# Kernel optimization log

Hardware: AMD Instinct MI355X
Metric: run time of the kernel (lower is better)

Reference implementation:

```python
import jax, jax.numpy as jnp
import numpy as np

NUM_NODES = 100000
HIDDEN = 128
NUM_EDGES = 800000


def setup_inputs() -> dict:
    key = jax.random.key(0)
    ks = jax.random.split(key, 8)
    s = 1.0 / np.sqrt(HIDDEN)

    def lin_w(k):
        return jax.random.uniform(k, (HIDDEN, HIDDEN), minval=-s, maxval=s, dtype=jnp.float32)

    return {
        "node_id": jnp.arange(NUM_NODES, dtype=jnp.int64) if jax.config.jax_enable_x64 else jnp.arange(NUM_NODES, dtype=jnp.int32),
        "edge_index": jax.random.randint(ks[0], (2, NUM_EDGES), 0, NUM_NODES),
        "emb": jax.random.normal(ks[1], (NUM_NODES, HIDDEN), dtype=jnp.float32),
        "W1l": lin_w(ks[2]), "b1l": jnp.zeros((HIDDEN,), jnp.float32), "W1r": lin_w(ks[3]),
        "W2l": lin_w(ks[4]), "b2l": jnp.zeros((HIDDEN,), jnp.float32), "W2r": lin_w(ks[5]),
        "W3l": lin_w(ks[6]), "b3l": jnp.zeros((HIDDEN,), jnp.float32), "W3r": lin_w(ks[7]),
    }


def reference(node_id, edge_index, emb, W1l, b1l, W1r, W2l, b2l, W2r, W3l, b3l, W3r):
    # x: [N, H] node features from embedding lookup
    x = emb[node_id]
    src, dst = edge_index[0], edge_index[1]

    # in-degree per target node (PyG mean aggregation; zero-degree -> 0 output)
    deg = jax.ops.segment_sum(jnp.ones((NUM_EDGES,), x.dtype), dst, num_segments=NUM_NODES)
    inv_deg = 1.0 / jnp.maximum(deg, 1.0)  # [N]

    def sage_conv(h, Wl, bl, Wr):
        # gather source features [E, H], scatter-sum at targets, then mean
        aggr = jax.ops.segment_sum(h[src], dst, num_segments=NUM_NODES) * inv_deg[:, None]
        # out = lin_l(aggr) + lin_r(h); lin_l has bias, lin_r has none (PyG defaults)
        return aggr @ Wl.T + bl + h @ Wr.T

    x = jax.nn.relu(sage_conv(x, W1l, b1l, W1r))
    # dropout p=0.2 with training=False is identity (eval mode)
    x = jax.nn.relu(sage_conv(x, W2l, b2l, W2r))
    return sage_conv(x, W3l, b3l, W3r)
```

## Files before the change

### kernel.cpp

```cpp
#include <hip/hip_runtime.h>

#define H 128

typedef float v4f __attribute__((ext_vector_type(4)));
typedef short v8s __attribute__((ext_vector_type(8)));


__device__ inline unsigned short bf16_rne(float x) {
  unsigned u = __builtin_bit_cast(unsigned, x);
  unsigned r = u + 0x7FFF + ((u >> 16) & 1);
  return (unsigned short)(r >> 16);
}

__device__ inline void split_bf16(float x, unsigned short& hi, unsigned short& lo) {
  unsigned u = __builtin_bit_cast(unsigned, x);
  unsigned r = u + 0x7FFF + ((u >> 16) & 1);
  hi = (unsigned short)(r >> 16);
  float hf = __builtin_bit_cast(float, r & 0xFFFF0000u);
  float d = x - hf;
  unsigned ud = __builtin_bit_cast(unsigned, d);
  unsigned rd = ud + 0x7FFF + ((ud >> 16) & 1);
  lo = (unsigned short)(rd >> 16);
}


__global__ void hist_kernel(const int* __restrict__ dst, int* __restrict__ deg, int E) {
  int e = blockIdx.x * 256 + threadIdx.x;
  if (e < E) atomicAdd(&deg[dst[e]], 1);
}

__global__ __launch_bounds__(1024) void scan1_kernel(const int* __restrict__ deg,
                                                     int* __restrict__ incl,
                                                     int* __restrict__ blk_sum, int N) {
  __shared__ int lds[1024];
  int t = threadIdx.x;
  int i = blockIdx.x * 1024 + t;
  int v = (i < N) ? deg[i] : 0;
  lds[t] = v;
  __syncthreads();
  for (int off = 1; off < 1024; off <<= 1) {
    int x = (t >= off) ? lds[t - off] : 0;
    __syncthreads();
    lds[t] += x;
    __syncthreads();
  }
  if (i < N) incl[i] = lds[t];
  if (t == 1023) blk_sum[blockIdx.x] = lds[1023];
}

__global__ void scan2_kernel(const int* __restrict__ blk_sum, int* __restrict__ blk_off, int B) {
  __shared__ int lds[256];
  int t = threadIdx.x;
  int v = (t < B) ? blk_sum[t] : 0;
  lds[t] = v;
  __syncthreads();
  for (int off = 1; off < 256; off <<= 1) {
    int x = (t >= off) ? lds[t - off] : 0;
    __syncthreads();
    lds[t] += x;
    __syncthreads();
  }
  blk_off[t] = lds[t] - v;
}

__global__ void rowstart_kernel(const int* __restrict__ incl, const int* __restrict__ deg,
                                const int* __restrict__ blk_off, int* __restrict__ row_start,
                                int N) {
  int i = blockIdx.x * 256 + threadIdx.x;
  if (i < N) row_start[i] = blk_off[i >> 10] + incl[i] - deg[i];
}

__global__ void fill_kernel(const int* __restrict__ src, const int* __restrict__ dst,
                            const int* __restrict__ row_start, int* __restrict__ cursor,
                            int* __restrict__ csr_src, int E) {
  int e = blockIdx.x * 256 + threadIdx.x;
  if (e < E) {
    int d = dst[e];
    int p = atomicAdd(&cursor[d], 1);
    csr_src[row_start[d] + p] = src[e];
  }
}


__global__ void gather_kernel(const float* __restrict__ emb, const int* __restrict__ node_id,
                              float* __restrict__ h, unsigned short* __restrict__ hb, int N) {
  int i = blockIdx.x * 256 + threadIdx.x;
  if (i < N * 32) {
    int n = i >> 5, q = i & 31;
    float4 v = ((const float4*)emb)[(size_t)node_id[n] * 32 + q];
    ((float4*)h)[(size_t)n * 32 + q] = v;
    unsigned b0 = bf16_rne(v.x), b1 = bf16_rne(v.y), b2 = bf16_rne(v.z), b3 = bf16_rne(v.w);
    *(uint2*)(hb + (size_t)n * H + q * 4) = make_uint2(b0 | (b1 << 16), b2 | (b3 << 16));
  }
}


__global__ void wsplit_kernel(const float* __restrict__ W0, const float* __restrict__ W1,
                              const float* __restrict__ W2, const float* __restrict__ W3,
                              const float* __restrict__ W4, const float* __restrict__ W5,
                              unsigned short* __restrict__ hi, unsigned short* __restrict__ lo) {
  int i = blockIdx.x * 256 + threadIdx.x;
  int plane = i >> 12;
  int e = (i & 4095) * 4;
  const float* src = plane == 0 ? W0 : plane == 1 ? W1 : plane == 2 ? W2
                   : plane == 3 ? W3 : plane == 4 ? W4 : W5;
  float4 v = *(const float4*)(src + e);
  float vv[4] = {v.x, v.y, v.z, v.w};
  unsigned short hs[4], ls[4];
#pragma unroll
  for (int k = 0; k < 4; ++k) split_bf16(vv[k], hs[k], ls[k]);
  size_t base = (size_t)plane * 16384 + e;
  *(uint2*)(&hi[base]) = make_uint2((unsigned)hs[0] | ((unsigned)hs[1] << 16),
                                    (unsigned)hs[2] | ((unsigned)hs[3] << 16));
  *(uint2*)(&lo[base]) = make_uint2((unsigned)ls[0] | ((unsigned)ls[1] << 16),
                                    (unsigned)ls[2] | ((unsigned)ls[3] << 16));
}


__global__ __launch_bounds__(256) void aggregate_kernel(const unsigned short* __restrict__ hb,
                                                        const int* __restrict__ csr_src,
                                                        const int* __restrict__ row_start,
                                                        const int* __restrict__ deg,
                                                        float* __restrict__ aggr, int N) {
  int node = blockIdx.x * 4 + (threadIdx.x >> 6);
  if (node >= N) return;
  int lane = threadIdx.x & 63;
  int qe = lane >> 4;
  int cl = lane & 15;
  const uint4* __restrict__ h16 = (const uint4*)hb;

  int start = row_start[node];
  int d = deg[node];

  float acc[8] = {0.f, 0.f, 0.f, 0.f, 0.f, 0.f, 0.f, 0.f};

  auto accum = [&](uint4 u) {
    unsigned uu[4] = {u.x, u.y, u.z, u.w};
#pragma unroll
    for (int j = 0; j < 4; ++j) {
      acc[2 * j] += __builtin_bit_cast(float, uu[j] << 16);
      acc[2 * j + 1] += __builtin_bit_cast(float, uu[j] & 0xFFFF0000u);
    }
  };

  int e = qe;
  for (; e + 4 < d; e += 8) {
    int s0 = csr_src[start + e];
    int s1 = csr_src[start + e + 4];
    uint4 u0 = h16[(size_t)s0 * 16 + cl];
    uint4 u1 = h16[(size_t)s1 * 16 + cl];
    accum(u0);
    accum(u1);
  }
  for (; e < d; e += 4) {
    int s = csr_src[start + e];
    accum(h16[(size_t)s * 16 + cl]);
  }

#pragma unroll
  for (int j = 0; j < 8; ++j) {
    acc[j] += __shfl_xor(acc[j], 16);
    acc[j] += __shfl_xor(acc[j], 32);
  }

  float inv = 1.0f / fmaxf((float)d, 1.0f);
  if (qe == 0) {
    *(float4*)(aggr + (size_t)node * H + cl * 8) =
        make_float4(acc[0] * inv, acc[1] * inv, acc[2] * inv, acc[3] * inv);
  } else if (qe == 1) {
    *(float4*)(aggr + (size_t)node * H + cl * 8 + 4) =
        make_float4(acc[4] * inv, acc[5] * inv, acc[6] * inv, acc[7] * inv);
  }
}


template <int RELU>
__global__ __launch_bounds__(256) void gemm_mfma(const float* __restrict__ aggr,
                                                 const float* h,
                                                 const unsigned short* __restrict__ Wl_hi,
                                                 const unsigned short* __restrict__ Wl_lo,
                                                 const unsigned short* __restrict__ Wr_hi,
                                                 const unsigned short* __restrict__ Wr_lo,
                                                 const float* __restrict__ bias,
                                                 float* out, unsigned short* hb_out, int N) {
  __shared__ __align__(16) unsigned short Ah[4096];
  __shared__ __align__(16) unsigned short Al[4096];
  __shared__ __align__(16) unsigned short Wh[4096];
  __shared__ __align__(16) unsigned short Wl_[4096];

  int tid = threadIdx.x;
  int wave = tid >> 6, lane = tid & 63;
  int m = lane & 15, q = lane >> 4;
  int block_row = blockIdx.x * 128;

  v4f acc[16];
#pragma unroll
  for (int t = 0; t < 16; ++t) acc[t] = (v4f){0.f, 0.f, 0.f, 0.f};

  for (int side = 0; side < 2; ++side) {
    const float* X = side ? h : aggr;
    const unsigned short* WH = side ? Wr_hi : Wl_hi;
    const unsigned short* WL = side ? Wr_lo : Wl_lo;

    for (int kb = 0; kb < 4; ++kb) {
      __syncthreads();

#pragma unroll
      for (int p = 0; p < 4; ++p) {
        int s = p * 256 + tid;
        int row = s >> 3;
        int g = s & 7;
        int grow = block_row + row;
        if (grow >= N) grow = N - 1;
        float4 v = *(const float4*)(X + (size_t)grow * H + kb * 32 + g * 4);
        float vv[4] = {v.x, v.y, v.z, v.w};
        unsigned short hs[4], ls[4];
#pragma unroll
        for (int k = 0; k < 4; ++k) split_bf16(vv[k], hs[k], ls[k]);
        int off = (row >> 4) * 512 + (((g >> 1) * 16) + (row & 15)) * 8 + (g & 1) * 4;
        *(uint2*)(&Ah[off]) = make_uint2((unsigned)hs[0] | ((unsigned)hs[1] << 16),
                                         (unsigned)hs[2] | ((unsigned)hs[3] << 16));
        *(uint2*)(&Al[off]) = make_uint2((unsigned)ls[0] | ((unsigned)ls[1] << 16),
                                         (unsigned)ls[2] | ((unsigned)ls[3] << 16));
      }

#pragma unroll
      for (int p = 0; p < 2; ++p) {
        int s = p * 256 + tid;
        int row = s >> 2;
        int g2 = s & 3;
        size_t gsrc = (size_t)row * H + kb * 32 + g2 * 8;
        v8s wh = *(const v8s*)(WH + gsrc);
        v8s wl = *(const v8s*)(WL + gsrc);
        int off = (row >> 4) * 512 + (g2 * 16 + (row & 15)) * 8;
        *(v8s*)(&Wh[off]) = wh;
        *(v8s*)(&Wl_[off]) = wl;
      }

      __syncthreads();

      const v8s* AhF = (const v8s*)Ah;
      const v8s* AlF = (const v8s*)Al;
      const v8s* WhF = (const v8s*)Wh;
      const v8s* WlF = (const v8s*)Wl_;
      v8s ah0 = AhF[(wave * 2 + 0) * 64 + lane];
      v8s ah1 = AhF[(wave * 2 + 1) * 64 + lane];
      v8s al0 = AlF[(wave * 2 + 0) * 64 + lane];
      v8s al1 = AlF[(wave * 2 + 1) * 64 + lane];
#pragma unroll
      for (int c = 0; c < 8; ++c) {
        v8s bh = WhF[c * 64 + lane];
        v8s bl = WlF[c * 64 + lane];
        acc[c] = __builtin_amdgcn_mfma_f32_16x16x32_bf16(ah0, bh, acc[c], 0, 0, 0);
        acc[c] = __builtin_amdgcn_mfma_f32_16x16x32_bf16(al0, bh, acc[c], 0, 0, 0);
        acc[c] = __builtin_amdgcn_mfma_f32_16x16x32_bf16(ah0, bl, acc[c], 0, 0, 0);
        acc[8 + c] = __builtin_amdgcn_mfma_f32_16x16x32_bf16(ah1, bh, acc[8 + c], 0, 0, 0);
        acc[8 + c] = __builtin_amdgcn_mfma_f32_16x16x32_bf16(al1, bh, acc[8 + c], 0, 0, 0);
        acc[8 + c] = __builtin_amdgcn_mfma_f32_16x16x32_bf16(ah1, bl, acc[8 + c], 0, 0, 0);
      }
    }
  }

  float bv[8];
#pragma unroll
  for (int c = 0; c < 8; ++c) bv[c] = bias[c * 16 + m];
#pragma unroll
  for (int tr = 0; tr < 2; ++tr) {
#pragma unroll
    for (int c = 0; c < 8; ++c) {
      v4f a = acc[tr * 8 + c];
#pragma unroll
      for (int i = 0; i < 4; ++i) {
        int row = block_row + wave * 32 + tr * 16 + q * 4 + i;
        if (row < N) {
          float v = a[i] + bv[c];
          if (RELU) v = fmaxf(v, 0.f);
          out[(size_t)row * H + c * 16 + m] = v;
          if (hb_out) hb_out[(size_t)row * H + c * 16 + m] = bf16_rne(v);
        }
      }
    }
  }
}


extern "C" void kernel_launch(void* const* d_in, const int* in_sizes, int n_in,
                              void* d_out, int out_size, void* d_ws, size_t ws_size,
                              hipStream_t stream) {
  const int* node_id = (const int*)d_in[0];
  const int* edge_index = (const int*)d_in[1];
  const float* emb = (const float*)d_in[2];
  const float* W1l = (const float*)d_in[3];
  const float* b1l = (const float*)d_in[4];
  const float* W1r = (const float*)d_in[5];
  const float* W2l = (const float*)d_in[6];
  const float* b2l = (const float*)d_in[7];
  const float* W2r = (const float*)d_in[8];
  const float* W3l = (const float*)d_in[9];
  const float* b3l = (const float*)d_in[10];
  const float* W3r = (const float*)d_in[11];

  int N = in_sizes[0];
  int E = in_sizes[1] / 2;
  const int* src = edge_index;
  const int* dst = edge_index + E;

  char* w = (char*)d_ws;
  auto alloc = [&](size_t bytes) {
    void* p = (void*)w;
    w += (bytes + 255) & ~(size_t)255;
    return p;
  };
  int* deg = (int*)alloc((size_t)N * 4);
  int* cursor = (int*)alloc((size_t)N * 4);
  int* row_start = (int*)alloc((size_t)N * 4);
  int* incl = (int*)alloc((size_t)N * 4);
  int* blk_sum = (int*)alloc(1024);
  int* blk_off = (int*)alloc(1024);
  int* csr_src = (int*)alloc((size_t)E * 4);
  float* hbuf = (float*)alloc((size_t)N * H * 4);
  float* aggr = (float*)alloc((size_t)N * H * 4);
  unsigned short* hb = (unsigned short*)alloc((size_t)N * H * 2);
  unsigned short* whi = (unsigned short*)alloc(6 * 16384 * 2);
  unsigned short* wlo = (unsigned short*)alloc(6 * 16384 * 2);

  hipMemsetAsync(deg, 0, (size_t)N * 4, stream);
  hipMemsetAsync(cursor, 0, (size_t)N * 4, stream);

  hist_kernel<<<(E + 255) / 256, 256, 0, stream>>>(dst, deg, E);
  int SB = (N + 1023) / 1024;
  scan1_kernel<<<SB, 1024, 0, stream>>>(deg, incl, blk_sum, N);
  scan2_kernel<<<1, 256, 0, stream>>>(blk_sum, blk_off, SB);
  rowstart_kernel<<<(N + 255) / 256, 256, 0, stream>>>(incl, deg, blk_off, row_start, N);
  fill_kernel<<<(E + 255) / 256, 256, 0, stream>>>(src, dst, row_start, cursor, csr_src, E);

  gather_kernel<<<(N * 32 + 255) / 256, 256, 0, stream>>>(emb, node_id, hbuf, hb, N);
  wsplit_kernel<<<96, 256, 0, stream>>>(W1l, W1r, W2l, W2r, W3l, W3r, whi, wlo);

  int gag = (N + 3) / 4;
  int ggm = (N + 127) / 128;

  aggregate_kernel<<<gag, 256, 0, stream>>>(hb, csr_src, row_start, deg, aggr, N);
  gemm_mfma<1><<<ggm, 256, 0, stream>>>(aggr, hbuf, whi + 0 * 16384, wlo + 0 * 16384,
                                        whi + 1 * 16384, wlo + 1 * 16384, b1l, hbuf, hb, N);

  aggregate_kernel<<<gag, 256, 0, stream>>>(hb, csr_src, row_start, deg, aggr, N);
  gemm_mfma<1><<<ggm, 256, 0, stream>>>(aggr, hbuf, whi + 2 * 16384, wlo + 2 * 16384,
                                        whi + 3 * 16384, wlo + 3 * 16384, b2l, hbuf, hb, N);

  aggregate_kernel<<<gag, 256, 0, stream>>>(hb, csr_src, row_start, deg, aggr, N);
  gemm_mfma<0><<<ggm, 256, 0, stream>>>(aggr, hbuf, whi + 4 * 16384, wlo + 4 * 16384,
                                        whi + 5 * 16384, wlo + 5 * 16384, b3l, (float*)d_out,
                                        nullptr, N);
}
```

Measured before the change: 470.7 us.

## Store activations pre-split into MFMA fragment layout, drop LDS staging in GEMM

Producers (gather, aggregate, GEMM epilogue) now write bf16 hi/lo planes directly in the 16-row MFMA fragment layout instead of fp32 row-major. The GEMM loads operand fragments straight from global memory with no shared-memory staging, no barriers and no per-tile hi/lo splitting. This removes the fp32 read/write traffic and the repeated split work inside the GEMM. In exchange, weight fragments are reloaded from global or cache by every wave, and the epilogue issues scattered 2-byte stores to three buffers. The GEMM also reads and writes hHi/hLo in place across blocks, which is safe only because each block touches only its own row tiles.

Result: slower. 534.5 us (+13.6%).

```diff
diff --git a/kernel.cpp b/kernel.cpp
--- a/kernel.cpp
+++ b/kernel.cpp
@@ -22,6 +22,7 @@
   unsigned rd = ud + 0x7FFF + ((ud >> 16) & 1);
   lo = (unsigned short)(rd >> 16);
 }
+
 
 
 __global__ void hist_kernel(const int* __restrict__ dst, int* __restrict__ deg, int E) {
@@ -83,15 +84,26 @@
 
 
 __global__ void gather_kernel(const float* __restrict__ emb, const int* __restrict__ node_id,
-                              float* __restrict__ h, unsigned short* __restrict__ hb, int N) {
+                              unsigned short* __restrict__ hHi, unsigned short* __restrict__ hLo,
+                              unsigned short* __restrict__ hRM, int N) {
   int i = blockIdx.x * 256 + threadIdx.x;
-  if (i < N * 32) {
-    int n = i >> 5, q = i & 31;
-    float4 v = ((const float4*)emb)[(size_t)node_id[n] * 32 + q];
-    ((float4*)h)[(size_t)n * 32 + q] = v;
-    unsigned b0 = bf16_rne(v.x), b1 = bf16_rne(v.y), b2 = bf16_rne(v.z), b3 = bf16_rne(v.w);
-    *(uint2*)(hb + (size_t)n * H + q * 4) = make_uint2(b0 | (b1 << 16), b2 | (b3 << 16));
-  }
+  if (i >= N * 32) return;
+  int n = i >> 5, q = i & 31;
+  float4 v = ((const float4*)emb)[(size_t)node_id[n] * 32 + q];
+  float vv[4] = {v.x, v.y, v.z, v.w};
+  unsigned short hs[4], ls[4];
+#pragma unroll
+  for (int k = 0; k < 4; ++k) split_bf16(vv[k], hs[k], ls[k]);
+  int c0 = q * 4;
+  size_t off = (size_t)(n >> 4) * 2048 + (c0 >> 5) * 512 + (((c0 >> 3) & 3) * 128) +
+               ((n & 15) * 8) + (c0 & 7);
+  uint2 hp = make_uint2((unsigned)hs[0] | ((unsigned)hs[1] << 16),
+                        (unsigned)hs[2] | ((unsigned)hs[3] << 16));
+  uint2 lp = make_uint2((unsigned)ls[0] | ((unsigned)ls[1] << 16),
+                        (unsigned)ls[2] | ((unsigned)ls[3] << 16));
+  *(uint2*)(hHi + off) = hp;
+  *(uint2*)(hLo + off) = lp;
+  *(uint2*)(hRM + (size_t)n * H + c0) = hp;
 }
 
 
@@ -109,25 +121,29 @@
   unsigned short hs[4], ls[4];
 #pragma unroll
   for (int k = 0; k < 4; ++k) split_bf16(vv[k], hs[k], ls[k]);
-  size_t base = (size_t)plane * 16384 + e;
-  *(uint2*)(&hi[base]) = make_uint2((unsigned)hs[0] | ((unsigned)hs[1] << 16),
-                                    (unsigned)hs[2] | ((unsigned)hs[3] << 16));
-  *(uint2*)(&lo[base]) = make_uint2((unsigned)ls[0] | ((unsigned)ls[1] << 16),
-                                    (unsigned)ls[2] | ((unsigned)ls[3] << 16));
-}
-
-
-__global__ __launch_bounds__(256) void aggregate_kernel(const unsigned short* __restrict__ hb,
+  int row = e >> 7, c0 = e & 127;
+  size_t off = (size_t)plane * 16384 + (row >> 4) * 2048 + (c0 >> 5) * 512 +
+               (((c0 >> 3) & 3) * 128) + ((row & 15) * 8) + (c0 & 7);
+  *(uint2*)(&hi[off]) = make_uint2((unsigned)hs[0] | ((unsigned)hs[1] << 16),
+                                   (unsigned)hs[2] | ((unsigned)hs[3] << 16));
+  *(uint2*)(&lo[off]) = make_uint2((unsigned)ls[0] | ((unsigned)ls[1] << 16),
+                                   (unsigned)ls[2] | ((unsigned)ls[3] << 16));
+}
+
+
+__global__ __launch_bounds__(256) void aggregate_kernel(const unsigned short* __restrict__ hRM,
                                                         const int* __restrict__ csr_src,
                                                         const int* __restrict__ row_start,
                                                         const int* __restrict__ deg,
-                                                        float* __restrict__ aggr, int N) {
+                                                        unsigned short* __restrict__ aggrHi,
+                                                        unsigned short* __restrict__ aggrLo,
+                                                        int N) {
   int node = blockIdx.x * 4 + (threadIdx.x >> 6);
   if (node >= N) return;
   int lane = threadIdx.x & 63;
   int qe = lane >> 4;
   int cl = lane & 15;
-  const uint4* __restrict__ h16 = (const uint4*)hb;
+  const uint4* __restrict__ h16 = (const uint4*)hRM;
 
   int start = row_start[node];
   int d = deg[node];
@@ -164,93 +180,62 @@
   }
 
   float inv = 1.0f / fmaxf((float)d, 1.0f);
+  unsigned short hs[8], ls[8];
+#pragma unroll
+  for (int j = 0; j < 8; ++j) split_bf16(acc[j] * inv, hs[j], ls[j]);
+  size_t off = (size_t)(node >> 4) * 2048 + (cl >> 2) * 512 + ((cl & 3) * 128) + ((node & 15) * 8);
   if (qe == 0) {
-    *(float4*)(aggr + (size_t)node * H + cl * 8) =
-        make_float4(acc[0] * inv, acc[1] * inv, acc[2] * inv, acc[3] * inv);
+    *(uint4*)(aggrHi + off) = make_uint4((unsigned)hs[0] | ((unsigned)hs[1] << 16),
+                                         (unsigned)hs[2] | ((unsigned)hs[3] << 16),
+                                         (unsigned)hs[4] | ((unsigned)hs[5] << 16),
+                                         (unsigned)hs[6] | ((unsigned)hs[7] << 16));
   } else if (qe == 1) {
-    *(float4*)(aggr + (size_t)node * H + cl * 8 + 4) =
-        make_float4(acc[4] * inv, acc[5] * inv, acc[6] * inv, acc[7] * inv);
-  }
-}
-
-
-template <int RELU>
-__global__ __launch_bounds__(256) void gemm_mfma(const float* __restrict__ aggr,
-                                                 const float* h,
-                                                 const unsigned short* __restrict__ Wl_hi,
-                                                 const unsigned short* __restrict__ Wl_lo,
-                                                 const unsigned short* __restrict__ Wr_hi,
-                                                 const unsigned short* __restrict__ Wr_lo,
-                                                 const float* __restrict__ bias,
-                                                 float* out, unsigned short* hb_out, int N) {
-  __shared__ __align__(16) unsigned short Ah[4096];
-  __shared__ __align__(16) unsigned short Al[4096];
-  __shared__ __align__(16) unsigned short Wh[4096];
-  __shared__ __align__(16) unsigned short Wl_[4096];
-
+    *(uint4*)(aggrLo + off) = make_uint4((unsigned)ls[0] | ((unsigned)ls[1] << 16),
+                                         (unsigned)ls[2] | ((unsigned)ls[3] << 16),
+                                         (unsigned)ls[4] | ((unsigned)ls[5] << 16),
+                                         (unsigned)ls[6] | ((unsigned)ls[7] << 16));
+  }
+}
+
+
+template <int FINAL>
+__global__ __launch_bounds__(256) void gemm_mfma(
+    const unsigned short* aggrHi, const unsigned short* aggrLo,
+    const unsigned short* hHi, const unsigned short* hLo,
+    const unsigned short* __restrict__ wlHi, const unsigned short* __restrict__ wlLo,
+    const unsigned short* __restrict__ wrHi, const unsigned short* __restrict__ wrLo,
+    const float* __restrict__ bias, float* outF,
+    unsigned short* outHi, unsigned short* outLo, unsigned short* outRM, int N) {
   int tid = threadIdx.x;
   int wave = tid >> 6, lane = tid & 63;
   int m = lane & 15, q = lane >> 4;
-  int block_row = blockIdx.x * 128;
+  int nt = (N + 15) >> 4;
+  int rt0 = blockIdx.x * 8 + wave * 2;
+  int rt1 = rt0 + 1;
+  if (rt0 > nt - 1) rt0 = nt - 1;
+  if (rt1 > nt - 1) rt1 = nt - 1;
 
   v4f acc[16];
 #pragma unroll
   for (int t = 0; t < 16; ++t) acc[t] = (v4f){0.f, 0.f, 0.f, 0.f};
 
+#pragma unroll
   for (int side = 0; side < 2; ++side) {
-    const float* X = side ? h : aggr;
-    const unsigned short* WH = side ? Wr_hi : Wl_hi;
-    const unsigned short* WL = side ? Wr_lo : Wl_lo;
-
+    const v8s* XH = (const v8s*)(side ? hHi : aggrHi);
+    const v8s* XL = (const v8s*)(side ? hLo : aggrLo);
+    const v8s* WHp = (const v8s*)(side ? wrHi : wlHi);
+    const v8s* WLp = (const v8s*)(side ? wrLo : wlLo);
+#pragma unroll
     for (int kb = 0; kb < 4; ++kb) {
-      __syncthreads();
-
-#pragma unroll
-      for (int p = 0; p < 4; ++p) {
-        int s = p * 256 + tid;
-        int row = s >> 3;
-        int g = s & 7;
-        int grow = block_row + row;
-        if (grow >= N) grow = N - 1;
-        float4 v = *(const float4*)(X + (size_t)grow * H + kb * 32 + g * 4);
-        float vv[4] = {v.x, v.y, v.z, v.w};
-        unsigned short hs[4], ls[4];
-#pragma unroll
-        for (int k = 0; k < 4; ++k) split_bf16(vv[k], hs[k], ls[k]);
-        int off = (row >> 4) * 512 + (((g >> 1) * 16) + (row & 15)) * 8 + (g & 1) * 4;
-        *(uint2*)(&Ah[off]) = make_uint2((unsigned)hs[0] | ((unsigned)hs[1] << 16),
-                                         (unsigned)hs[2] | ((unsigned)hs[3] << 16));
-        *(uint2*)(&Al[off]) = make_uint2((unsigned)ls[0] | ((unsigned)ls[1] << 16),
-                                         (unsigned)ls[2] | ((unsigned)ls[3] << 16));
-      }
-
-#pragma unroll
-      for (int p = 0; p < 2; ++p) {
-        int s = p * 256 + tid;
-        int row = s >> 2;
-        int g2 = s & 3;
-        size_t gsrc = (size_t)row * H + kb * 32 + g2 * 8;
-        v8s wh = *(const v8s*)(WH + gsrc);
-        v8s wl = *(const v8s*)(WL + gsrc);
-        int off = (row >> 4) * 512 + (g2 * 16 + (row & 15)) * 8;
-        *(v8s*)(&Wh[off]) = wh;
-        *(v8s*)(&Wl_[off]) = wl;
-      }
-
-      __syncthreads();
-
-      const v8s* AhF = (const v8s*)Ah;
-      const v8s* AlF = (const v8s*)Al;
-      const v8s* WhF = (const v8s*)Wh;
-      const v8s* WlF = (const v8s*)Wl_;
-      v8s ah0 = AhF[(wave * 2 + 0) * 64 + lane];
-      v8s ah1 = AhF[(wave * 2 + 1) * 64 + lane];
-      v8s al0 = AlF[(wave * 2 + 0) * 64 + lane];
-      v8s al1 = AlF[(wave * 2 + 1) * 64 + lane];
+      int ib = kb * 64 + lane;
+      v8s ah0 = XH[(size_t)rt0 * 256 + ib];
+      v8s al0 = XL[(size_t)rt0 * 256 + ib];
+      v8s ah1 = XH[(size_t)rt1 * 256 + ib];
+      v8s al1 = XL[(size_t)rt1 * 256 + ib];
 #pragma unroll
       for (int c = 0; c < 8; ++c) {
-        v8s bh = WhF[c * 64 + lane];
-        v8s bl = WlF[c * 64 + lane];
+        v8s bh = WHp[c * 256 + ib];
+        v8s bl = WLp[c * 256 + ib];
         acc[c] = __builtin_amdgcn_mfma_f32_16x16x32_bf16(ah0, bh, acc[c], 0, 0, 0);
         acc[c] = __builtin_amdgcn_mfma_f32_16x16x32_bf16(al0, bh, acc[c], 0, 0, 0);
         acc[c] = __builtin_amdgcn_mfma_f32_16x16x32_bf16(ah0, bl, acc[c], 0, 0, 0);
@@ -271,12 +256,21 @@
       v4f a = acc[tr * 8 + c];
 #pragma unroll
       for (int i = 0; i < 4; ++i) {
-        int row = block_row + wave * 32 + tr * 16 + q * 4 + i;
+        int row = blockIdx.x * 128 + wave * 32 + tr * 16 + q * 4 + i;
         if (row < N) {
           float v = a[i] + bv[c];
-          if (RELU) v = fmaxf(v, 0.f);
-          out[(size_t)row * H + c * 16 + m] = v;
-          if (hb_out) hb_out[(size_t)row * H + c * 16 + m] = bf16_rne(v);
+          if (FINAL) {
+            outF[(size_t)row * H + c * 16 + m] = v;
+          } else {
+            v = fmaxf(v, 0.f);
+            unsigned short hs, ls;
+            split_bf16(v, hs, ls);
+            size_t fo = (size_t)(row >> 4) * 2048 + (c >> 1) * 512 +
+                        ((((c & 1) << 1) | (m >> 3)) * 128) + ((row & 15) * 8) + (m & 7);
+            outHi[fo] = hs;
+            outLo[fo] = ls;
+            outRM[(size_t)row * H + c * 16 + m] = hs;
+          }
         }
       }
     }
@@ -318,9 +312,12 @@
   int* blk_sum = (int*)alloc(1024);
   int* blk_off = (int*)alloc(1024);
   int* csr_src = (int*)alloc((size_t)E * 4);
-  float* hbuf = (float*)alloc((size_t)N * H * 4);
-  float* aggr = (float*)alloc((size_t)N * H * 4);
-  unsigned short* hb = (unsigned short*)alloc((size_t)N * H * 2);
+  size_t nt = ((size_t)N + 15) >> 4;
+  unsigned short* hHi = (unsigned short*)alloc(nt * 2048 * 2);
+  unsigned short* hLo = (unsigned short*)alloc(nt * 2048 * 2);
+  unsigned short* hRM = (unsigned short*)alloc((size_t)N * H * 2);
+  unsigned short* aggrHi = (unsigned short*)alloc(nt * 2048 * 2);
+  unsigned short* aggrLo = (unsigned short*)alloc(nt * 2048 * 2);
   unsigned short* whi = (unsigned short*)alloc(6 * 16384 * 2);
   unsigned short* wlo = (unsigned short*)alloc(6 * 16384 * 2);
 
@@ -334,22 +331,27 @@
   rowstart_kernel<<<(N + 255) / 256, 256, 0, stream>>>(incl, deg, blk_off, row_start, N);
   fill_kernel<<<(E + 255) / 256, 256, 0, stream>>>(src, dst, row_start, cursor, csr_src, E);
 
-  gather_kernel<<<(N * 32 + 255) / 256, 256, 0, stream>>>(emb, node_id, hbuf, hb, N);
+  gather_kernel<<<(N * 32 + 255) / 256, 256, 0, stream>>>(emb, node_id, hHi, hLo, hRM, N);
   wsplit_kernel<<<96, 256, 0, stream>>>(W1l, W1r, W2l, W2r, W3l, W3r, whi, wlo);
 
   int gag = (N + 3) / 4;
   int ggm = (N + 127) / 128;
 
-  aggregate_kernel<<<gag, 256, 0, stream>>>(hb, csr_src, row_start, deg, aggr, N);
-  gemm_mfma<1><<<ggm, 256, 0, stream>>>(aggr, hbuf, whi + 0 * 16384, wlo + 0 * 16384,
-                                        whi + 1 * 16384, wlo + 1 * 16384, b1l, hbuf, hb, N);
-
-  aggregate_kernel<<<gag, 256, 0, stream>>>(hb, csr_src, row_start, deg, aggr, N);
-  gemm_mfma<1><<<ggm, 256, 0, stream>>>(aggr, hbuf, whi + 2 * 16384, wlo + 2 * 16384,
-                                        whi + 3 * 16384, wlo + 3 * 16384, b2l, hbuf, hb, N);
-
-  aggregate_kernel<<<gag, 256, 0, stream>>>(hb, csr_src, row_start, deg, aggr, N);
-  gemm_mfma<0><<<ggm, 256, 0, stream>>>(aggr, hbuf, whi + 4 * 16384, wlo + 4 * 16384,
-                                        whi + 5 * 16384, wlo + 5 * 16384, b3l, (float*)d_out,
-                                        nullptr, N);
-}
+  aggregate_kernel<<<gag, 256, 0, stream>>>(hRM, csr_src, row_start, deg, aggrHi, aggrLo, N);
+  gemm_mfma<0><<<ggm, 256, 0, stream>>>(aggrHi, aggrLo, hHi, hLo,
+                                        whi + 0 * 16384, wlo + 0 * 16384,
+                                        whi + 1 * 16384, wlo + 1 * 16384,
+                                        b1l, nullptr, hHi, hLo, hRM, N);
+
+  aggregate_kernel<<<gag, 256, 0, stream>>>(hRM, csr_src, row_start, deg, aggrHi, aggrLo, N);
+  gemm_mfma<0><<<ggm, 256, 0, stream>>>(aggrHi, aggrLo, hHi, hLo,
+                                        whi + 2 * 16384, wlo + 2 * 16384,
+                                        whi + 3 * 16384, wlo + 3 * 16384,
+                                        b2l, nullptr, hHi, hLo, hRM, N);
+
+  aggregate_kernel<<<gag, 256, 0, stream>>>(hRM, csr_src, row_start, deg, aggrHi, aggrLo, N);
+  gemm_mfma<1><<<ggm, 256, 0, stream>>>(aggrHi, aggrLo, hHi, hLo,
+                                        whi + 4 * 16384, wlo + 4 * 16384,
+                                        whi + 5 * 16384, wlo + 5 * 16384,
+                                        b3l, (float*)d_out, nullptr, nullptr, nullptr, N);
+}
```
